# Kernel optimization log

Hardware: AMD Instinct MI355X
Metric: run time of the kernel (lower is better)

## Reference

```python
import jax, jax.numpy as jnp
import numpy as np

B, D_IN, D_HID, D_OUT, E = 8192, 1024, 4096, 1024, 8


def setup_inputs() -> dict:
    key = jax.random.key(0)
    ks = jax.random.split(key, 6)
    s_in = 1.0 / np.sqrt(D_IN)
    s_gh = 1.0 / np.sqrt(D_HID // 2)
    s_eh = 1.0 / np.sqrt(D_HID)
    return {
        "x": jax.random.normal(ks[0], (B, D_IN), jnp.float32),
        "gW1": jax.random.normal(ks[1], (D_IN, D_HID // 2), jnp.float32) * s_in,
        "gb1": jnp.zeros((D_HID // 2,), jnp.float32),
        "gW2": jax.random.normal(ks[2], (D_HID // 2, E), jnp.float32) * s_gh,
        "gb2": jnp.zeros((E,), jnp.float32),
        "eW1": jax.random.normal(ks[3], (E, D_IN, D_HID), jnp.float32) * s_in,
        "eb1": jnp.zeros((E, D_HID), jnp.float32),
        "eW2": jax.random.normal(ks[4], (E, D_HID, D_OUT), jnp.float32) * s_eh,
        "eb2": jnp.zeros((E, D_OUT), jnp.float32),
    }


def reference(x, gW1, gb1, gW2, gb2, eW1, eb1, eW2, eb2):
    # Gating network: Linear -> ReLU -> (Dropout: eval identity) -> Linear -> Softmax(dim=1)
    gh = jax.nn.relu(x @ gW1 + gb1)                      # [B, H/2]
    gates = jax.nn.softmax(gh @ gW2 + gb2, axis=1)       # [B, E]

    # All experts run on the full batch (dense MoE): batched GEMMs over expert axis.
    h = jax.nn.relu(jnp.einsum('bi,eih->beh', x, eW1) + eb1)   # [B, E, H]
    eo = jnp.einsum('beh,eho->beo', h, eW2) + eb2              # [B, E, O]

    # Gated weighted sum over experts.
    combined = jnp.einsum('beo,be->bo', eo, gates)             # [B, O]
    return (combined, gates, gates)
```

## Files before the change

### kernel.cpp

```cpp
#include <hip/hip_runtime.h>
#include <hip/hip_bf16.h>
#include <stdint.h>

#define BB 8192
#define DIN 1024
#define DHID 4096
#define DOUT 1024
#define NEXP 8
#define GH_N 2048

typedef __attribute__((ext_vector_type(8))) __bf16 bf16x8;
typedef __attribute__((ext_vector_type(4))) float f32x4;

__device__ inline unsigned short f2bf(float f) {
  unsigned u = __builtin_bit_cast(unsigned, f);
  u = (u + 0x7FFFu + ((u >> 16) & 1u)) >> 16;
  return (unsigned short)u;
}
__device__ inline float b2f(unsigned short s) {
  return __builtin_bit_cast(float, (unsigned)s << 16);
}

__global__ void cvt_f32_bf16(const float* __restrict__ in,
                             unsigned short* __restrict__ out, int n4) {
  int i = blockIdx.x * blockDim.x + threadIdx.x;
  if (i >= n4) return;
  float4 v = ((const float4*)in)[i];
  ushort4 o;
  o.x = f2bf(v.x); o.y = f2bf(v.y); o.z = f2bf(v.z); o.w = f2bf(v.w);
  ((ushort4*)out)[i] = o;
}

__device__ inline void tr_tile64(const float* __restrict__ in,
                                 unsigned short* __restrict__ out, int R, int C,
                                 int bx, int by) {
  __shared__ float tile[64][65];
  const int c0 = bx * 64, r0 = by * 64;
  const int tx = threadIdx.x & 63, ty = threadIdx.x >> 6;
#pragma unroll
  for (int i = 0; i < 16; ++i) {
    int r = i * 4 + ty;
    tile[r][tx] = in[(size_t)(r0 + r) * C + c0 + tx];
  }
  __syncthreads();
#pragma unroll
  for (int i = 0; i < 16; ++i) {
    int r = i * 4 + ty;
    out[(size_t)(c0 + r) * R + r0 + tx] = f2bf(tile[tx][r]);
  }
}

__global__ void transpose_cvt64(const float* __restrict__ in,
                                unsigned short* __restrict__ out, int R, int C) {
  tr_tile64(in, out, R, C, blockIdx.x, blockIdx.y);
}

__global__ void transpose_cvt2(const float* __restrict__ w1,
                               unsigned short* __restrict__ w1T,
                               const float* __restrict__ w2,
                               unsigned short* __restrict__ w2T) {
  int b = blockIdx.x;
  if (b < 1024) {
    tr_tile64(w1, w1T, DIN, DHID, b & 63, b >> 6);
  } else {
    b -= 1024;
    tr_tile64(w2, w2T, DHID, DOUT, b & 15, b >> 4);
  }
}

__device__ inline void gload16(const void* g, void* l) {
  __builtin_amdgcn_global_load_lds(
      (const __attribute__((address_space(1))) void*)g,
      (__attribute__((address_space(3))) void*)l, 16, 0, 0);
}

template <int N>
__device__ inline void waitv() {
  if constexpr (N == 0) asm volatile("s_waitcnt vmcnt(0)" ::: "memory");
  else if constexpr (N == 2) asm volatile("s_waitcnt vmcnt(2)" ::: "memory");
  else if constexpr (N == 4) asm volatile("s_waitcnt vmcnt(4)" ::: "memory");
  else asm volatile("s_waitcnt vmcnt(0)" ::: "memory");
}
__device__ inline void waitlgkm0() {
  asm volatile("s_waitcnt lgkmcnt(0)" ::: "memory");
  __builtin_amdgcn_sched_barrier(0);
}
__device__ inline bf16x8 ldr(const char* p) { return *(const bf16x8*)p; }

struct GArgs {
  const unsigned short* A;
  const unsigned short* Bt;
  int lda, ldb, N, K;
  const float* bias;
  unsigned short* outb;
  float* outf;
  const float* gates;
  int eidx, epi, nb;
};

__global__ __launch_bounds__(512, 2)
void gemmU(GArgs g) {
  __shared__ char lds[131072];
  char* Als = lds;
  char* Bls = lds + 65536;
  constexpr int ABYTES = 32768, BBYTES = 32768;
  const int t = threadIdx.x;
  const int lane = t & 63;
  const int wid = t >> 6;
  const int wm = wid >> 2;
  const int wn = wid & 3;
  const int l15 = lane & 15, lg = lane >> 4;

  const int nb = g.nb;
  const int local = blockIdx.x;
  const int swz = (local & 7) * (nb >> 3) + (local >> 3);
  int ks = 0, tid = swz;
  if (g.epi == 3) { ks = swz & 1; tid = swz >> 1; }
  const int nbn = g.N >> 8;
  const int bn = tid % nbn, bm = tid / nbn;
  const int m0 = bm * 256, n0 = bn * 256;
  const int kbase = ks * g.K;

  const int prow = t >> 3;
  const int cOff = ((t & 7) ^ (prow & 7)) * 8;
  const unsigned short* aP[4];
  const unsigned short* bP[4];
#pragma unroll
  for (int u = 0; u < 4; ++u) {
    int p = u * 64 + prow;
    int ga = ((p >> 6) & 1) * 128 + ((p >> 7) & 1) * 64 + (p & 63);
    aP[u] = g.A + (size_t)(m0 + ga) * g.lda + kbase + cOff;
    int gb = ((p >> 5) & 3) * 64 + ((p >> 7) & 1) * 32 + (p & 31);
    bP[u] = g.Bt + (size_t)(n0 + gb) * g.ldb + kbase + cOff;
  }
  const int ldst = t * 16;

  const int slot0 = ((lg) ^ (l15 & 7)) * 16;
  const int slot1 = ((4 + lg) ^ (l15 & 7)) * 16;
  const int aRB0 = (wm * 64 + l15) * 128;
  const int aRB1 = (128 + wm * 64 + l15) * 128;
  const int bCB0 = (wn * 32 + l15) * 128;
  const int bCB1 = (128 + wn * 32 + l15) * 128;

  f32x4 acc[8][4];
  const f32x4 zero = {0.f, 0.f, 0.f, 0.f};
#pragma unroll
  for (int i = 0; i < 8; ++i)
#pragma unroll
    for (int j = 0; j < 4; ++j) acc[i][j] = zero;

  bf16x8 ar[4][2], bc0[2][2], bc1[2][2];
  const int NT = g.K >> 6;

  gload16(bP[0], Bls + 0 * 8192 + ldst);
  gload16(bP[1], Bls + 1 * 8192 + ldst);
  gload16(aP[0], Als + 0 * 8192 + ldst);
  gload16(aP[1], Als + 1 * 8192 + ldst);
  gload16(bP[2], Bls + 2 * 8192 + ldst);
  gload16(bP[3], Bls + 3 * 8192 + ldst);
  gload16(aP[2], Als + 2 * 8192 + ldst);
  gload16(aP[3], Als + 3 * 8192 + ldst);
  waitv<4>();
  __builtin_amdgcn_s_barrier();

  for (int T = 0; T < NT; ++T) {
    const int buf = T & 1;
    const char* Ab = Als + buf * ABYTES;
    const char* Bb = Bls + buf * BBYTES;
    char* An = Als + (buf ^ 1) * ABYTES;
    char* Bn = Bls + (buf ^ 1) * BBYTES;
    const bool stg = (T + 1 < NT);
    const int kn = (T + 1) << 6;

#pragma unroll
    for (int f = 0; f < 4; ++f) {
      ar[f][0] = ldr(Ab + aRB0 + f * 2048 + slot0);
      ar[f][1] = ldr(Ab + aRB0 + f * 2048 + slot1);
    }
#pragma unroll
    for (int c = 0; c < 2; ++c) {
      bc0[c][0] = ldr(Bb + bCB0 + c * 2048 + slot0);
      bc0[c][1] = ldr(Bb + bCB0 + c * 2048 + slot1);
    }
    if (stg) {
      gload16(bP[0] + kn, Bn + 0 * 8192 + ldst);
      gload16(bP[1] + kn, Bn + 1 * 8192 + ldst);
    }
    __builtin_amdgcn_s_barrier();
    waitlgkm0();
    __builtin_amdgcn_s_setprio(1);
#pragma unroll
    for (int ksl = 0; ksl < 2; ++ksl)
#pragma unroll
      for (int f = 0; f < 4; ++f)
#pragma unroll
        for (int c = 0; c < 2; ++c)
          acc[f][c] = __builtin_amdgcn_mfma_f32_16x16x32_bf16(
              ar[f][ksl], bc0[c][ksl], acc[f][c], 0, 0, 0);
    __builtin_amdgcn_s_setprio(0);
    if (stg) waitv<4>(); else waitv<2>();
    __builtin_amdgcn_s_barrier();

#pragma unroll
    for (int c = 0; c < 2; ++c) {
      bc1[c][0] = ldr(Bb + bCB1 + c * 2048 + slot0);
      bc1[c][1] = ldr(Bb + bCB1 + c * 2048 + slot1);
    }
    if (stg) {
      gload16(aP[0] + kn, An + 0 * 8192 + ldst);
      gload16(aP[1] + kn, An + 1 * 8192 + ldst);
    }
    __builtin_amdgcn_s_barrier();
    waitlgkm0();
    __builtin_amdgcn_s_setprio(1);
#pragma unroll
    for (int ksl = 0; ksl < 2; ++ksl)
#pragma unroll
      for (int f = 0; f < 4; ++f)
#pragma unroll
        for (int c = 0; c < 2; ++c)
          acc[f][2 + c] = __builtin_amdgcn_mfma_f32_16x16x32_bf16(
              ar[f][ksl], bc1[c][ksl], acc[f][2 + c], 0, 0, 0);
    __builtin_amdgcn_s_setprio(0);
    if (stg) waitv<4>(); else waitv<0>();
    __builtin_amdgcn_s_barrier();

#pragma unroll
    for (int f = 0; f < 4; ++f) {
      ar[f][0] = ldr(Ab + aRB1 + f * 2048 + slot0);
      ar[f][1] = ldr(Ab + aRB1 + f * 2048 + slot1);
    }
    if (stg) {
      gload16(bP[2] + kn, Bn + 2 * 8192 + ldst);
      gload16(bP[3] + kn, Bn + 3 * 8192 + ldst);
    }
    __builtin_amdgcn_s_barrier();
    waitlgkm0();
    __builtin_amdgcn_s_setprio(1);
#pragma unroll
    for (int ksl = 0; ksl < 2; ++ksl)
#pragma unroll
      for (int f = 0; f < 4; ++f)
#pragma unroll
        for (int c = 0; c < 2; ++c)
          acc[4 + f][2 + c] = __builtin_amdgcn_mfma_f32_16x16x32_bf16(
              ar[f][ksl], bc1[c][ksl], acc[4 + f][2 + c], 0, 0, 0);
    __builtin_amdgcn_s_setprio(0);
    __builtin_amdgcn_s_barrier();

    if (stg) {
      gload16(aP[2] + kn, An + 2 * 8192 + ldst);
      gload16(aP[3] + kn, An + 3 * 8192 + ldst);
    }
    __builtin_amdgcn_s_barrier();
    __builtin_amdgcn_s_setprio(1);
#pragma unroll
    for (int ksl = 0; ksl < 2; ++ksl)
#pragma unroll
      for (int f = 0; f < 4; ++f)
#pragma unroll
        for (int c = 0; c < 2; ++c)
          acc[4 + f][c] = __builtin_amdgcn_mfma_f32_16x16x32_bf16(
              ar[f][ksl], bc0[c][ksl], acc[4 + f][c], 0, 0, 0);
    __builtin_amdgcn_s_setprio(0);
    if (stg) waitv<4>();
    __builtin_amdgcn_s_barrier();
  }

  const int rb = m0 + wm * 128 + (lg << 2);
  const int cb = n0 + wn * 64 + l15;
  const int N = g.N;
  if (g.epi == 0) {
#pragma unroll
    for (int fg = 0; fg < 8; ++fg) {
#pragma unroll
      for (int j = 0; j < 4; ++j) {
        int col = cb + j * 16;
        float bv = g.bias[col];
#pragma unroll
        for (int r = 0; r < 4; ++r) {
          int row = rb + fg * 16 + r;
          float v = acc[fg][j][r] + bv;
          g.outb[(size_t)row * N + col] = f2bf(fmaxf(v, 0.f));
        }
      }
    }
  } else {
#pragma unroll
    for (int fg = 0; fg < 8; ++fg) {
      float gv[4];
#pragma unroll
      for (int r = 0; r < 4; ++r)
        gv[r] = g.gates[(size_t)(rb + fg * 16 + r) * NEXP + g.eidx];
#pragma unroll
      for (int j = 0; j < 4; ++j) {
        int col = cb + j * 16;
#pragma unroll
        for (int r = 0; r < 4; ++r) {
          size_t o = (size_t)(rb + fg * 16 + r) * N + col;
          __hip_atomic_fetch_add(&g.outf[o], acc[fg][j][r] * gv[r],
                                 __ATOMIC_RELAXED, __HIP_MEMORY_SCOPE_AGENT);
        }
      }
    }
  }
}

__global__ void init_c(const float* __restrict__ gat,
                       const float* __restrict__ eb2,
                       float* __restrict__ outC) {
  const int r = blockIdx.x;
  const int c4 = threadIdx.x;
  float g[8];
#pragma unroll
  for (int e = 0; e < 8; ++e) g[e] = gat[(size_t)r * NEXP + e];
  float4 o = {0.f, 0.f, 0.f, 0.f};
#pragma unroll
  for (int e = 0; e < 8; ++e) {
    float4 b = ((const float4*)(eb2 + (size_t)e * DOUT))[c4];
    o.x += g[e] * b.x; o.y += g[e] * b.y;
    o.z += g[e] * b.z; o.w += g[e] * b.w;
  }
  ((float4*)(outC + (size_t)r * DOUT))[c4] = o;
}

__global__ __launch_bounds__(512)
void gating_head2(const unsigned short* __restrict__ gh,
                  const float* __restrict__ gW2,
                  const float* __restrict__ gb2,
                  float* __restrict__ gws,
                  float* __restrict__ g1,
                  float* __restrict__ g2) {
  __shared__ float wT[8][2048];
  const int t = threadIdx.x;
  for (int idx = t; idx < 16384; idx += 512) {
    wT[idx & 7][idx >> 3] = gW2[idx];
  }
  __syncthreads();
  const int wid = t >> 6, lane = t & 63;
  const int row = blockIdx.x * 8 + wid;
  const unsigned short* ghr = gh + (size_t)row * 2048;
  float s[8] = {0.f, 0.f, 0.f, 0.f, 0.f, 0.f, 0.f, 0.f};
#pragma unroll
  for (int j = 0; j < 8; ++j) {
    int k4 = lane + 64 * j;
    ushort4 hv = ((const ushort4*)ghr)[k4];
    float h0 = b2f(hv.x), h1 = b2f(hv.y), h2 = b2f(hv.z), h3 = b2f(hv.w);
#pragma unroll
    for (int e = 0; e < 8; ++e) {
      float4 w = ((const float4*)&wT[e][0])[k4];
      s[e] += h0 * w.x + h1 * w.y + h2 * w.z + h3 * w.w;
    }
  }
#pragma unroll
  for (int e = 0; e < 8; ++e)
#pragma unroll
    for (int off = 1; off < 64; off <<= 1) s[e] += __shfl_xor(s[e], off, 64);
  if (lane == 0) {
    float l[8], m = -1e30f;
#pragma unroll
    for (int e = 0; e < 8; ++e) {
      l[e] = s[e] + gb2[e];
      m = fmaxf(m, l[e]);
    }
    float sum = 0.f;
#pragma unroll
    for (int e = 0; e < 8; ++e) {
      l[e] = expf(l[e] - m);
      sum += l[e];
    }
    float inv = 1.f / sum;
#pragma unroll
    for (int e = 0; e < 8; ++e) {
      float gv = l[e] * inv;
      gws[(size_t)row * 8 + e] = gv;
      g1[(size_t)row * 8 + e] = gv;
      g2[(size_t)row * 8 + e] = gv;
    }
  }
}

extern "C" void kernel_launch(void* const* d_in, const int* in_sizes, int n_in,
                              void* d_out, int out_size, void* d_ws,
                              size_t ws_size, hipStream_t stream) {
  (void)in_sizes; (void)n_in; (void)out_size; (void)ws_size;
  const float* x   = (const float*)d_in[0];
  const float* gW1 = (const float*)d_in[1];
  const float* gb1 = (const float*)d_in[2];
  const float* gW2 = (const float*)d_in[3];
  const float* gb2 = (const float*)d_in[4];
  const float* eW1 = (const float*)d_in[5];
  const float* eb1 = (const float*)d_in[6];
  const float* eW2 = (const float*)d_in[7];
  const float* eb2 = (const float*)d_in[8];

  float* outC  = (float*)d_out;
  float* outG1 = outC + (size_t)BB * DOUT;
  float* outG2 = outG1 + (size_t)BB * NEXP;

  char* ws = (char*)d_ws;
  unsigned short* xb   = (unsigned short*)(ws);
  float*          gat  = (float*)(ws + 16777216);
  unsigned short* w1T  = (unsigned short*)(ws + 17039360);
  unsigned short* w2T  = (unsigned short*)(ws + 25427968);
  unsigned short* hbuf = (unsigned short*)(ws + 33816576);
  unsigned short* gh   = hbuf;
  unsigned short* gW1T = w1T;

  cvt_f32_bf16<<<(BB * DIN / 4) / 256, 256, 0, stream>>>(x, xb, BB * DIN / 4);
  transpose_cvt64<<<dim3(GH_N / 64, DIN / 64), 256, 0, stream>>>(gW1, gW1T, DIN, GH_N);
  {
    GArgs a{xb, gW1T, DIN, DIN, GH_N, DIN, gb1, gh, nullptr, nullptr, 0, 0, 256};
    gemmU<<<256, 512, 0, stream>>>(a);
  }
  gating_head2<<<BB / 8, 512, 0, stream>>>(gh, gW2, gb2, gat, outG1, outG2);
  init_c<<<BB, 256, 0, stream>>>(gat, eb2, outC);

  for (int e = 0; e < NEXP; ++e) {
    transpose_cvt2<<<2048, 256, 0, stream>>>(
        eW1 + (size_t)e * DIN * DHID, w1T, eW2 + (size_t)e * DHID * DOUT, w2T);
    {
      GArgs a{xb, w1T, DIN, DIN, DHID, DIN, eb1 + (size_t)e * DHID,
              hbuf, nullptr, nullptr, 0, 0, 512};
      gemmU<<<512, 512, 0, stream>>>(a);
    }
    {
      GArgs a{hbuf, w2T, DHID, DHID, DOUT, DHID / 2, nullptr, nullptr,
              outC, gat, e, 3, 256};
      gemmU<<<256, 512, 0, stream>>>(a);
    }
  }
}
```

Before: 1.551 ms.

## Replace split-K atomic second GEMM with full-K 128x256 tile kernel using plain stores

The second expert GEMM, which used split-K by 2 with atomic fp32 adds into the output, is replaced by a dedicated kernel. It computes the full K=4096 with 128x256 tiles and a 3-stage LDS ring. It adds the bias and gate scaling in its epilogue and writes or accumulates the output with ordinary loads and stores, ordered across experts by the stream. This removes the atomics and the separate init_c kernel. The costs are a longer K loop per block with 256 blocks at smaller tiles, a read-modify-write of the output for each expert, and a different LDS footprint and occupancy.

```diff
diff --git a/kernel.cpp b/kernel.cpp
--- a/kernel.cpp
+++ b/kernel.cpp
@@ -79,6 +79,7 @@
   if constexpr (N == 0) asm volatile("s_waitcnt vmcnt(0)" ::: "memory");
   else if constexpr (N == 2) asm volatile("s_waitcnt vmcnt(2)" ::: "memory");
   else if constexpr (N == 4) asm volatile("s_waitcnt vmcnt(4)" ::: "memory");
+  else if constexpr (N == 6) asm volatile("s_waitcnt vmcnt(6)" ::: "memory");
   else asm volatile("s_waitcnt vmcnt(0)" ::: "memory");
 }
 __device__ inline void waitlgkm0() {
@@ -93,9 +94,7 @@
   int lda, ldb, N, K;
   const float* bias;
   unsigned short* outb;
-  float* outf;
-  const float* gates;
-  int eidx, epi, nb;
+  int nb;
 };
 
 __global__ __launch_bounds__(512, 2)
@@ -114,12 +113,9 @@
   const int nb = g.nb;
   const int local = blockIdx.x;
   const int swz = (local & 7) * (nb >> 3) + (local >> 3);
-  int ks = 0, tid = swz;
-  if (g.epi == 3) { ks = swz & 1; tid = swz >> 1; }
   const int nbn = g.N >> 8;
-  const int bn = tid % nbn, bm = tid / nbn;
+  const int bn = swz % nbn, bm = swz / nbn;
   const int m0 = bm * 256, n0 = bn * 256;
-  const int kbase = ks * g.K;
 
   const int prow = t >> 3;
   const int cOff = ((t & 7) ^ (prow & 7)) * 8;
@@ -129,9 +125,9 @@
   for (int u = 0; u < 4; ++u) {
     int p = u * 64 + prow;
     int ga = ((p >> 6) & 1) * 128 + ((p >> 7) & 1) * 64 + (p & 63);
-    aP[u] = g.A + (size_t)(m0 + ga) * g.lda + kbase + cOff;
+    aP[u] = g.A + (size_t)(m0 + ga) * g.lda + cOff;
     int gb = ((p >> 5) & 3) * 64 + ((p >> 7) & 1) * 32 + (p & 31);
-    bP[u] = g.Bt + (size_t)(n0 + gb) * g.ldb + kbase + cOff;
+    bP[u] = g.Bt + (size_t)(n0 + gb) * g.ldb + cOff;
   }
   const int ldst = t * 16;
 
@@ -270,58 +266,171 @@
   const int rb = m0 + wm * 128 + (lg << 2);
   const int cb = n0 + wn * 64 + l15;
   const int N = g.N;
-  if (g.epi == 0) {
-#pragma unroll
-    for (int fg = 0; fg < 8; ++fg) {
-#pragma unroll
-      for (int j = 0; j < 4; ++j) {
-        int col = cb + j * 16;
-        float bv = g.bias[col];
-#pragma unroll
-        for (int r = 0; r < 4; ++r) {
-          int row = rb + fg * 16 + r;
-          float v = acc[fg][j][r] + bv;
-          g.outb[(size_t)row * N + col] = f2bf(fmaxf(v, 0.f));
-        }
+#pragma unroll
+  for (int fg = 0; fg < 8; ++fg) {
+#pragma unroll
+    for (int j = 0; j < 4; ++j) {
+      int col = cb + j * 16;
+      float bv = g.bias[col];
+#pragma unroll
+      for (int r = 0; r < 4; ++r) {
+        int row = rb + fg * 16 + r;
+        float v = acc[fg][j][r] + bv;
+        g.outb[(size_t)row * N + col] = f2bf(fmaxf(v, 0.f));
       }
     }
-  } else {
-#pragma unroll
-    for (int fg = 0; fg < 8; ++fg) {
-      float gv[4];
-#pragma unroll
-      for (int r = 0; r < 4; ++r)
-        gv[r] = g.gates[(size_t)(rb + fg * 16 + r) * NEXP + g.eidx];
-#pragma unroll
-      for (int j = 0; j < 4; ++j) {
-        int col = cb + j * 16;
-#pragma unroll
-        for (int r = 0; r < 4; ++r) {
-          size_t o = (size_t)(rb + fg * 16 + r) * N + col;
-          __hip_atomic_fetch_add(&g.outf[o], acc[fg][j][r] * gv[r],
-                                 __ATOMIC_RELAXED, __HIP_MEMORY_SCOPE_AGENT);
-        }
+  }
+}
+
+__global__ __launch_bounds__(512)
+void gemmF(const unsigned short* __restrict__ A,
+           const unsigned short* __restrict__ Bt,
+           const float* __restrict__ bias,
+           float* __restrict__ outC,
+           const float* __restrict__ gates, int eidx, int accum) {
+  constexpr int SLOT = 49152;
+  __shared__ char lds[3 * SLOT];
+  const int t = threadIdx.x;
+  const int lane = t & 63;
+  const int wid = t >> 6;
+  const int wm = wid >> 2;
+  const int wn = wid & 3;
+  const int l15 = lane & 15, lg = lane >> 4;
+
+  const int local = blockIdx.x;
+  const int swz = (local & 7) * 32 + (local >> 3);
+  const int bn = swz & 3, bm = swz >> 2;
+  const int m0 = bm * 128, n0 = bn * 256;
+
+  const int prow = t >> 3;
+  const int cOff = ((t & 7) ^ (prow & 7)) * 8;
+  const unsigned short* aP[2];
+  const unsigned short* bP[4];
+#pragma unroll
+  for (int u = 0; u < 2; ++u)
+    aP[u] = A + (size_t)(m0 + u * 64 + prow) * DHID + cOff;
+#pragma unroll
+  for (int u = 0; u < 4; ++u) {
+    int p = u * 64 + prow;
+    int gb = ((p >> 5) & 3) * 64 + ((p >> 7) & 1) * 32 + (p & 31);
+    bP[u] = Bt + (size_t)(n0 + gb) * DHID + cOff;
+  }
+  const int ldst = t * 16;
+
+  const int slot0 = ((lg) ^ (l15 & 7)) * 16;
+  const int slot1 = ((4 + lg) ^ (l15 & 7)) * 16;
+  const int aRB = (wm * 64 + l15) * 128;
+  const int bCB0 = 16384 + (wn * 32 + l15) * 128;
+  const int bCB1 = 16384 + (128 + wn * 32 + l15) * 128;
+
+  f32x4 acc[4][4];
+  const f32x4 zero = {0.f, 0.f, 0.f, 0.f};
+#pragma unroll
+  for (int i = 0; i < 4; ++i)
+#pragma unroll
+    for (int j = 0; j < 4; ++j) acc[i][j] = zero;
+
+  bf16x8 af[2][2], bc[4][2];
+  const int NT = DHID >> 6;
+
+#pragma unroll
+  for (int T0 = 0; T0 < 2; ++T0) {
+    char* S = lds + T0 * SLOT;
+    const int k0 = T0 << 6;
+    gload16(aP[0] + k0, S + 0 * 8192 + ldst);
+    gload16(aP[1] + k0, S + 1 * 8192 + ldst);
+    gload16(bP[0] + k0, S + 16384 + 0 * 8192 + ldst);
+    gload16(bP[1] + k0, S + 16384 + 1 * 8192 + ldst);
+    gload16(bP[2] + k0, S + 16384 + 2 * 8192 + ldst);
+    gload16(bP[3] + k0, S + 16384 + 3 * 8192 + ldst);
+  }
+  waitv<6>();
+  __builtin_amdgcn_s_barrier();
+
+  for (int T = 0; T < NT; ++T) {
+    const char* Sb = lds + (T % 3) * SLOT;
+    char* Sn = lds + ((T + 2) % 3) * SLOT;
+    const bool stg = (T + 2 < NT);
+    const int kn = (T + 2) << 6;
+
+#pragma unroll
+    for (int f = 0; f < 2; ++f) {
+      af[f][0] = ldr(Sb + aRB + f * 2048 + slot0);
+      af[f][1] = ldr(Sb + aRB + f * 2048 + slot1);
+    }
+#pragma unroll
+    for (int c = 0; c < 2; ++c) {
+      bc[c][0] = ldr(Sb + bCB0 + c * 2048 + slot0);
+      bc[c][1] = ldr(Sb + bCB0 + c * 2048 + slot1);
+      bc[2 + c][0] = ldr(Sb + bCB1 + c * 2048 + slot0);
+      bc[2 + c][1] = ldr(Sb + bCB1 + c * 2048 + slot1);
+    }
+    if (stg) {
+      gload16(aP[0] + kn, Sn + 0 * 8192 + ldst);
+      gload16(aP[1] + kn, Sn + 1 * 8192 + ldst);
+      gload16(bP[0] + kn, Sn + 16384 + 0 * 8192 + ldst);
+    }
+    __builtin_amdgcn_s_barrier();
+    waitlgkm0();
+    __builtin_amdgcn_s_setprio(1);
+#pragma unroll
+    for (int ksl = 0; ksl < 2; ++ksl)
+#pragma unroll
+      for (int f = 0; f < 2; ++f)
+#pragma unroll
+        for (int c = 0; c < 4; ++c)
+          acc[f][c] = __builtin_amdgcn_mfma_f32_16x16x32_bf16(
+              af[f][ksl], bc[c][ksl], acc[f][c], 0, 0, 0);
+    __builtin_amdgcn_s_setprio(0);
+    __builtin_amdgcn_s_barrier();
+
+#pragma unroll
+    for (int f = 0; f < 2; ++f) {
+      af[f][0] = ldr(Sb + aRB + (2 + f) * 2048 + slot0);
+      af[f][1] = ldr(Sb + aRB + (2 + f) * 2048 + slot1);
+    }
+    if (stg) {
+      gload16(bP[1] + kn, Sn + 16384 + 1 * 8192 + ldst);
+      gload16(bP[2] + kn, Sn + 16384 + 2 * 8192 + ldst);
+      gload16(bP[3] + kn, Sn + 16384 + 3 * 8192 + ldst);
+    }
+    __builtin_amdgcn_s_barrier();
+    waitlgkm0();
+    __builtin_amdgcn_s_setprio(1);
+#pragma unroll
+    for (int ksl = 0; ksl < 2; ++ksl)
+#pragma unroll
+      for (int f = 0; f < 2; ++f)
+#pragma unroll
+        for (int c = 0; c < 4; ++c)
+          acc[2 + f][c] = __builtin_amdgcn_mfma_f32_16x16x32_bf16(
+              af[f][ksl], bc[c][ksl], acc[2 + f][c], 0, 0, 0);
+    __builtin_amdgcn_s_setprio(0);
+    if (stg) waitv<6>();
+    else if (T + 1 < NT) waitv<0>();
+    __builtin_amdgcn_s_barrier();
+  }
+
+  const int rb = m0 + wm * 64 + (lg << 2);
+  const int cb = n0 + wn * 64 + l15;
+#pragma unroll
+  for (int fg = 0; fg < 4; ++fg) {
+    float gv[4];
+#pragma unroll
+    for (int r = 0; r < 4; ++r)
+      gv[r] = gates[(size_t)(rb + fg * 16 + r) * NEXP + eidx];
+#pragma unroll
+    for (int j = 0; j < 4; ++j) {
+      int col = cb + j * 16;
+      float bv = bias[col];
+#pragma unroll
+      for (int r = 0; r < 4; ++r) {
+        size_t o = (size_t)(rb + fg * 16 + r) * DOUT + col;
+        float v = (acc[fg][j][r] + bv) * gv[r];
+        outC[o] = accum ? outC[o] + v : v;
       }
     }
   }
-}
-
-__global__ void init_c(const float* __restrict__ gat,
-                       const float* __restrict__ eb2,
-                       float* __restrict__ outC) {
-  const int r = blockIdx.x;
-  const int c4 = threadIdx.x;
-  float g[8];
-#pragma unroll
-  for (int e = 0; e < 8; ++e) g[e] = gat[(size_t)r * NEXP + e];
-  float4 o = {0.f, 0.f, 0.f, 0.f};
-#pragma unroll
-  for (int e = 0; e < 8; ++e) {
-    float4 b = ((const float4*)(eb2 + (size_t)e * DOUT))[c4];
-    o.x += g[e] * b.x; o.y += g[e] * b.y;
-    o.z += g[e] * b.z; o.w += g[e] * b.w;
-  }
-  ((float4*)(outC + (size_t)r * DOUT))[c4] = o;
 }
 
 __global__ __launch_bounds__(512)
@@ -410,24 +519,19 @@
   cvt_f32_bf16<<<(BB * DIN / 4) / 256, 256, 0, stream>>>(x, xb, BB * DIN / 4);
   transpose_cvt64<<<dim3(GH_N / 64, DIN / 64), 256, 0, stream>>>(gW1, gW1T, DIN, GH_N);
   {
-    GArgs a{xb, gW1T, DIN, DIN, GH_N, DIN, gb1, gh, nullptr, nullptr, 0, 0, 256};
+    GArgs a{xb, gW1T, DIN, DIN, GH_N, DIN, gb1, gh, 256};
     gemmU<<<256, 512, 0, stream>>>(a);
   }
   gating_head2<<<BB / 8, 512, 0, stream>>>(gh, gW2, gb2, gat, outG1, outG2);
-  init_c<<<BB, 256, 0, stream>>>(gat, eb2, outC);
 
   for (int e = 0; e < NEXP; ++e) {
     transpose_cvt2<<<2048, 256, 0, stream>>>(
         eW1 + (size_t)e * DIN * DHID, w1T, eW2 + (size_t)e * DHID * DOUT, w2T);
     {
-      GArgs a{xb, w1T, DIN, DIN, DHID, DIN, eb1 + (size_t)e * DHID,
-              hbuf, nullptr, nullptr, 0, 0, 512};
+      GArgs a{xb, w1T, DIN, DIN, DHID, DIN, eb1 + (size_t)e * DHID, hbuf, 512};
       gemmU<<<512, 512, 0, stream>>>(a);
     }
-    {
-      GArgs a{hbuf, w2T, DHID, DHID, DOUT, DHID / 2, nullptr, nullptr,
-              outC, gat, e, 3, 256};
-      gemmU<<<256, 512, 0, stream>>>(a);
-    }
-  }
-}
+    gemmF<<<256, 512, 0, stream>>>(hbuf, w2T, eb2 + (size_t)e * DOUT, outC,
+                                   gat, e, e > 0 ? 1 : 0);
+  }
+}
```

Result: faster. 1.343 ms (-13.5%).
